# Kernel optimization log

Measured on AMD Instinct MI355X. Metric: run time of the kernel, lower is better.

The kernel has to match this reference:

```python
import jax, jax.numpy as jnp
import numpy as np
import math

B, N, C = 1, 2048, 256
H, CH = 8, 32
PQ, PV = 8, 12
CZ = 32
BQ, BK = 32, 128
NB = N // BQ
PAD = (BK - BQ) // 2
INF = 1e8
EPS = 1e-8

_KIDX = np.arange(NB)[:, None] * BQ + np.arange(BK)[None, :] - PAD
_KVALID = (_KIDX >= 0) & (_KIDX < N)
_KIDX_C = np.clip(_KIDX, 0, N - 1)


def _quat_to_rot(q):
    q = q / jnp.linalg.norm(q, axis=-1, keepdims=True)
    w, x, y, z = q[..., 0], q[..., 1], q[..., 2], q[..., 3]
    return jnp.stack([
        jnp.stack([1 - 2 * (y * y + z * z), 2 * (x * y - w * z), 2 * (x * z + w * y)], -1),
        jnp.stack([2 * (x * y + w * z), 1 - 2 * (x * x + z * z), 2 * (y * z - w * x)], -1),
        jnp.stack([2 * (x * z - w * y), 2 * (y * z + w * x), 1 - 2 * (x * x + y * y)], -1)], -2)


def _to_queries(x):
    # [B, N, ...] -> [B, NB, BQ, ...]
    return x.reshape((B, NB, BQ) + x.shape[2:])


def _to_keys(x):
    # [B, N, ...] -> [B, NB, BK, ...] zero-padded sliding key windows
    g = x[:, _KIDX_C]
    v = jnp.asarray(_KVALID, x.dtype).reshape((1, NB, BK) + (1,) * (x.ndim - 2))
    return g * v


def _ln(x):
    m = x.mean(-1, keepdims=True)
    var = x.var(-1, keepdims=True)
    return (x - m) / jnp.sqrt(var + 1e-5)


def setup_inputs():
    key = jax.random.key(0)
    ks = jax.random.split(key, 16)
    p = 0.02
    return {
        's': jax.random.normal(ks[0], (B, N, C), jnp.float32),
        'cond': jax.random.normal(ks[1], (B, N, C), jnp.float32),
        'z': jax.random.normal(ks[2], (B, NB, BQ, BK, CZ), jnp.float32),
        'trans': jax.random.normal(ks[3], (B, N, 3), jnp.float32),
        'rots': _quat_to_rot(jax.random.normal(ks[4], (B, N, 4), jnp.float32)),
        's_mask': jnp.ones((B, N), jnp.float32),
        'Wq': jax.random.normal(ks[5], (C, H * CH)) * p,
        'Wk': jax.random.normal(ks[6], (C, H * CH)) * p,
        'Wv': jax.random.normal(ks[7], (C, H * CH)) * p,
        'Wqp': jax.random.normal(ks[8], (C, H * PQ * 3)) * p,
        'Wkvp': jax.random.normal(ks[9], (C, H * (PQ + PV) * 3)) * p,
        'Wb': jax.random.normal(ks[10], (CZ, H)) * p,
        'Wdz': jax.random.normal(ks[11], (CZ, CZ // 4)) * p,
        'head_weights': jnp.full((H,), 0.5413),
        'Wout': jax.random.normal(ks[12], (H * (CZ // 4 + CH + PV * 4), C)) * p,
        'Wg': jax.random.normal(ks[13], (C, C)) * p,
        'bg': jnp.zeros((C,)),
        'Wbeta': jax.random.normal(ks[14], (C, C)) * p,
        'bbeta': jnp.zeros((C,)),
        'g_z': jnp.ones((CZ,)),
        'b_z': jnp.zeros((CZ,)),
    }


def reference(s, cond, z, trans, rots, s_mask, Wq, Wk, Wv, Wqp, Wkvp, Wb, Wdz,
              head_weights, Wout, Wg, bg, Wbeta, bbeta, g_z, b_z):
    # AdaLN on s conditioned on cond; LayerNorm on z
    s = _ln(s) * (cond @ Wg + bg) + (cond @ Wbeta + bbeta)
    z = _ln(z) * g_z + b_z

    q_in = _to_queries(s)            # [B,NB,BQ,C]
    k_in = _to_keys(s)               # [B,NB,BK,C]
    q_t = _to_queries(trans)         # [B,NB,BQ,3]
    q_R = _to_queries(rots)          # [B,NB,BQ,3,3]
    k_t = _to_keys(trans)
    k_R = _to_keys(rots)
    # zero-padded key rotations -> identity
    zero = jnp.all(k_R == 0, axis=(-2, -1))[..., None, None]
    k_R = jnp.where(zero, jnp.eye(3, dtype=k_R.dtype), k_R)

    q = (q_in @ Wq).reshape(B, NB, BQ, H, CH)
    k = (k_in @ Wk).reshape(B, NB, BK, H, CH)
    v = (k_in @ Wv).reshape(B, NB, BK, H, CH)

    q_pts = (q_in @ Wqp).reshape(B, NB, BQ, H * PQ, 3)
    q_pts = jnp.einsum('bnqij,bnqpj->bnqpi', q_R, q_pts) + q_t[..., None, :]
    q_pts = q_pts.reshape(B, NB, BQ, H, PQ, 3)

    kv_pts = (k_in @ Wkvp).reshape(B, NB, BK, H * (PQ + PV), 3)
    kv_pts = jnp.einsum('bnkij,bnkpj->bnkpi', k_R, kv_pts) + k_t[..., None, :]
    kv_pts = kv_pts.reshape(B, NB, BK, H, PQ + PV, 3)
    k_pts, v_pts = kv_pts[..., :PQ, :], kv_pts[..., PQ:, :]

    b = z @ Wb                                    # [B,NB,BQ,BK,H]
    a = jnp.einsum('bnqhc,bnkhc->bnqkh', q, k) * math.sqrt(1.0 / (3 * CH))
    a = a + math.sqrt(1.0 / 3.0) * b

    disp = q_pts[:, :, :, None] - k_pts[:, :, None]   # [B,NB,BQ,BK,H,PQ,3]
    d2 = jnp.sum(disp * disp, axis=-1)                # [B,NB,BQ,BK,H,PQ]
    hw = jax.nn.softplus(head_weights) * math.sqrt(1.0 / (3 * (PQ * 9.0 / 2)))
    pt_att = -0.5 * jnp.sum(d2 * hw[:, None], axis=-1)   # [B,NB,BQ,BK,H]

    m_q = _to_queries(s_mask[..., None])              # [B,NB,BQ,1]
    m_k = _to_keys(s_mask[..., None])                 # [B,NB,BK,1]
    attn_mask = m_q * jnp.swapaxes(m_k, -1, -2)       # [B,NB,BQ,BK]
    attn_mask = INF * (attn_mask - 1.0)

    a = a + pt_att + attn_mask[..., None]
    a = jnp.swapaxes(a, -1, -2)                       # [B,NB,BQ,H,BK]
    a = jax.nn.softmax(a, axis=-1)

    o = jnp.einsum('bnqhk,bnkhc->bnqhc', a, v).reshape(B, NB, BQ, H * CH)
    o_pt = jnp.einsum('bnqhk,bnkhvc->bnqhvc', a, v_pts)      # [B,NB,BQ,H,PV,3]
    o_pt = jnp.einsum('bnqji,bnqhvj->bnqhvi', q_R,
                      o_pt - q_t[:, :, :, None, None, :])     # invert apply
    o_pt_norm = jnp.sqrt(jnp.sum(o_pt ** 2, -1) + EPS).reshape(B, NB, BQ, H * PV)
    o_pt = o_pt.reshape(B, NB, BQ, H * PV * 3)
    pair_z = z @ Wdz                                          # [B,NB,BQ,BK,CZ//4]
    o_pair = jnp.einsum('bnqhk,bnqkc->bnqhc', a, pair_z).reshape(B, NB, BQ, H * (CZ // 4))

    out = jnp.concatenate([o, o_pt, o_pt_norm, o_pair], -1) @ Wout
    return out.reshape(B, N, C)
```

## Files before the change

kernel.cpp:

```cpp
#include <hip/hip_runtime.h>
#include <hip/hip_bf16.h>
#include <math.h>

typedef __hip_bfloat16 bf16;
typedef __attribute__((ext_vector_type(8))) short short8;
typedef __attribute__((ext_vector_type(4))) short short4v;
typedef __attribute__((ext_vector_type(4))) float f32x4;

#define NRES 2048
#define CDIM 256
#define PADK 48
#define POS 1440

static __device__ __forceinline__ float b2f(bf16 x) { return __bfloat162float(x); }
static __device__ __forceinline__ float us2f(short u) {
    return __uint_as_float(((unsigned)(unsigned short)u) << 16);
}
static __device__ __forceinline__ short f2s(float f) {
    bf16 h = __float2bfloat16(f);
    return *reinterpret_cast<short*>(&h);
}
static __device__ __forceinline__ bool flag_f32(const void* smask) {
    return *(const unsigned int*)smask == 0x3F800000u;
}
static __device__ __forceinline__ float dual_load(const void* p, size_t i, bool f32) {
    float vf = ((const float*)p)[f32 ? i : 0];
    float vb = b2f(((const bf16*)p)[f32 ? (size_t)0 : i]);
    return f32 ? vf : vb;
}

struct PrepTable {
    const void* src[8];
    bf16* dst[8];
    int srcN[8];
    int nOff[8];
    int dstStride[8];
    float scl[8];
    int tileOff[9];
    const void* s;
    const void* cond;
    bf16* condb;
    bf16* xnb;
    const void* rots;
    const void* trans;
    float* RT;
    const void* z;
    const void* Wb;
    const void* Wdz;
    const void* g_z;
    const void* b_z;
    bf16* Bzb;
    bf16* PZb;
};
__global__ __launch_bounds__(256) void k_prep(PrepTable tb, const void* __restrict__ smask) {
    __shared__ float tile[32][33];
    __shared__ float ls[8][CDIM];
    __shared__ float mrs[8][2];
    __shared__ float wb[32][8], wdz[32][8], gz[32], bz[32];
    bool f32 = flag_f32(smask);
    int b = blockIdx.x;
    int t = threadIdx.x;
    if (b < 1024) {
        {
            int j = t >> 3, c = t & 7;
            wb[j][c] = 0.5773502691896258f * dual_load(tb.Wb, t, f32);
            wdz[j][c] = dual_load(tb.Wdz, t, f32);
        }
        if (t < 32) { gz[t] = dual_load(tb.g_z, t, f32); bz[t] = dual_load(tb.b_z, t, f32); }
        __syncthreads();
        size_t r = (size_t)b * 256 + t;
        float zv[32];
        float sum = 0.f, sq = 0.f;
        if (f32) {
            const float4* zp = (const float4*)((const float*)tb.z + r * 32);
#pragma unroll
            for (int j4 = 0; j4 < 8; ++j4) {
                float4 v4 = zp[j4];
                zv[j4 * 4 + 0] = v4.x; zv[j4 * 4 + 1] = v4.y; zv[j4 * 4 + 2] = v4.z; zv[j4 * 4 + 3] = v4.w;
            }
        } else {
            const bf16* zp = (const bf16*)tb.z + r * 32;
#pragma unroll
            for (int j = 0; j < 32; ++j) zv[j] = b2f(zp[j]);
        }
#pragma unroll
        for (int j = 0; j < 32; ++j) { float v = zv[j]; sum += v; sq += v * v; }
        float m = sum / 32.f;
        float var = fmaxf(sq / 32.f - m * m, 0.f);
        float rstd = rsqrtf(var + 1e-5f);
#pragma unroll
        for (int j = 0; j < 32; ++j) zv[j] = (zv[j] - m) * rstd * gz[j] + bz[j];
        float bacc[8], pacc[8];
#pragma unroll
        for (int c = 0; c < 8; ++c) { bacc[c] = 0.f; pacc[c] = 0.f; }
        for (int j = 0; j < 32; ++j) {
            float v = zv[j];
#pragma unroll
            for (int c = 0; c < 8; ++c) { bacc[c] += v * wb[j][c]; pacc[c] += v * wdz[j][c]; }
        }
        int n = (int)(r >> 12);
        int q = (int)(r >> 7) & 31;
        int k = (int)r & 127;
#pragma unroll
        for (int h = 0; h < 8; ++h)
            tb.Bzb[(size_t)n * 32768 + (size_t)h * 4096 + q * 128 + k] = __float2bfloat16(bacc[h]);
#pragma unroll
        for (int c = 0; c < 8; ++c)
            tb.PZb[(((size_t)(n * 32 + q)) * 8 + c) * 128 + k] = __float2bfloat16(pacc[c]);
        return;
    }
    b -= 1024;
    if (b < tb.tileOff[8]) {
        int s = 0;
        while (b >= tb.tileOff[s + 1]) ++s;
        int rel = b - tb.tileOff[s];
        int ntTiles = tb.srcN[s] >> 5;
        int kt = rel / ntTiles, nt = rel % ntTiles;
        const void* src = tb.src[s];
        int srcN = tb.srcN[s];
        float scl = tb.scl[s];
        int tx = t & 31, ty = t >> 5;
#pragma unroll
        for (int r = 0; r < 4; ++r) {
            int srow = kt * 32 + ty + r * 8;
            int scol = nt * 32 + tx;
            tile[ty + r * 8][tx] = dual_load(src, (size_t)srow * srcN + scol, f32);
        }
        __syncthreads();
        bf16* dst = tb.dst[s];
#pragma unroll
        for (int r = 0; r < 4; ++r) {
            int n = nt * 32 + ty + r * 8 + tb.nOff[s];
            int k = kt * 32 + tx;
            dst[(size_t)n * tb.dstStride[s] + k] = __float2bfloat16(tile[tx][ty + r * 8] * scl);
        }
        return;
    }
    b -= tb.tileOff[8];
    if (b < 256) {
        int i0 = b * 2048;
        for (int i = t; i < 2048; i += 256)
            tb.condb[i0 + i] = __float2bfloat16(dual_load(tb.cond, (size_t)(i0 + i), f32));
        return;
    }
    b -= 256;
    if (b < 256) {
        int r0 = b * 8;
        for (int i = t; i < 8 * CDIM; i += 256) {
            int r = i >> 8, c = i & 255;
            ls[r][c] = dual_load(tb.s, (size_t)(r0 + r) * CDIM + c, f32);
        }
        __syncthreads();
        int wave = t >> 6, lane = t & 63;
        for (int rr = 0; rr < 2; ++rr) {
            int r = wave * 2 + rr;
            float sum = 0.f, sq = 0.f;
            for (int j = lane; j < CDIM; j += 64) { float v = ls[r][j]; sum += v; sq += v * v; }
            for (int off = 32; off; off >>= 1) { sum += __shfl_xor(sum, off); sq += __shfl_xor(sq, off); }
            if (lane == 0) {
                float m = sum / CDIM;
                float var = fmaxf(sq / CDIM - m * m, 0.f);
                mrs[r][0] = m; mrs[r][1] = rsqrtf(var + 1e-5f);
            }
        }
        __syncthreads();
        int c = t;
#pragma unroll
        for (int r = 0; r < 8; ++r)
            tb.xnb[(size_t)(r0 + r) * CDIM + c] = __float2bfloat16((ls[r][c] - mrs[r][0]) * mrs[r][1]);
        return;
    }
    b -= 256;
    int i = b * 256 + t;
    int row = i / 12, c = i % 12;
    float v = (c < 9) ? dual_load(tb.rots, (size_t)row * 9 + c, f32)
                      : dual_load(tb.trans, (size_t)row * 3 + (c - 9), f32);
    tb.RT[i] = v;
}

__global__ __launch_bounds__(256) void k_gb(
    const bf16* __restrict__ condb, const bf16* __restrict__ GWt, const bf16* __restrict__ xnb,
    const void* __restrict__ bg, const void* __restrict__ bbeta,
    const void* __restrict__ smask, bf16* __restrict__ SQb)
{
    bool f32 = flag_f32(smask);
    int wid = threadIdx.x >> 6, lane = threadIdx.x & 63;
    int tid = blockIdx.x * 4 + wid;
    int mt = tid >> 4, nt = tid & 15;
    int idx = lane & 15, quad = lane >> 4;
    const bf16* Ap = condb + (size_t)(mt * 16 + idx) * 256 + quad * 8;
    const bf16* B0 = GWt + (size_t)(nt * 16 + idx) * 256 + quad * 8;
    const bf16* B1 = GWt + (size_t)(256 + nt * 16 + idx) * 256 + quad * 8;
    f32x4 a0 = {0,0,0,0}, a1 = {0,0,0,0};
    for (int k = 0; k < 256; k += 32) {
        short8 af = *(const short8*)(Ap + k);
        a0 = __builtin_amdgcn_mfma_f32_16x16x32_bf16(af, *(const short8*)(B0 + k), a0, 0, 0, 0);
        a1 = __builtin_amdgcn_mfma_f32_16x16x32_bf16(af, *(const short8*)(B1 + k), a1, 0, 0, 0);
    }
    int ocol = nt * 16 + idx;
    float bgc = dual_load(bg, ocol, f32), bbc = dual_load(bbeta, ocol, f32);
    int orow = mt * 16 + quad * 4;
#pragma unroll
    for (int r = 0; r < 4; ++r) {
        int row = orow + r;
        float xn = b2f(xnb[(size_t)row * 256 + ocol]);
        SQb[(size_t)row * 256 + ocol] = __float2bfloat16(xn * (a0[r] + bgc) + (a1[r] + bbc));
    }
}

__global__ __launch_bounds__(256) void k_gemm22b(
    const bf16* __restrict__ A, const bf16* __restrict__ Bt, bf16* __restrict__ C,
    int N, int K, int totalWaves)
{
    int wid = threadIdx.x >> 6, lane = threadIdx.x & 63;
    int tid = blockIdx.x * 4 + wid;
    if (tid >= totalWaves) return;
    int tiles_n = N >> 5;
    int mt = tid / tiles_n, nt = tid % tiles_n;
    int idx = lane & 15, quad = lane >> 4;
    const bf16* Ap0 = A + (size_t)(mt * 32 + idx) * K + quad * 8;
    const bf16* Ap1 = Ap0 + (size_t)16 * K;
    const bf16* Bp0 = Bt + (size_t)(nt * 32 + idx) * K + quad * 8;
    const bf16* Bp1 = Bp0 + (size_t)16 * K;
    f32x4 a00 = {0,0,0,0}, a01 = {0,0,0,0}, a10 = {0,0,0,0}, a11 = {0,0,0,0};
    for (int k = 0; k < K; k += 32) {
        short8 af0 = *(const short8*)(Ap0 + k);
        short8 af1 = *(const short8*)(Ap1 + k);
        short8 bf0 = *(const short8*)(Bp0 + k);
        short8 bf1 = *(const short8*)(Bp1 + k);
        a00 = __builtin_amdgcn_mfma_f32_16x16x32_bf16(af0, bf0, a00, 0, 0, 0);
        a01 = __builtin_amdgcn_mfma_f32_16x16x32_bf16(af0, bf1, a01, 0, 0, 0);
        a10 = __builtin_amdgcn_mfma_f32_16x16x32_bf16(af1, bf0, a10, 0, 0, 0);
        a11 = __builtin_amdgcn_mfma_f32_16x16x32_bf16(af1, bf1, a11, 0, 0, 0);
    }
    int orow = mt * 32 + quad * 4;
    int ocol = nt * 32 + idx;
#pragma unroll
    for (int r = 0; r < 4; ++r) {
        C[(size_t)(orow + r) * N + ocol] = __float2bfloat16(a00[r]);
        C[(size_t)(orow + r) * N + ocol + 16] = __float2bfloat16(a01[r]);
        C[(size_t)(orow + r + 16) * N + ocol] = __float2bfloat16(a10[r]);
        C[(size_t)(orow + r + 16) * N + ocol + 16] = __float2bfloat16(a11[r]);
    }
}

__global__ __launch_bounds__(256) void k_attn_out(
    const bf16* __restrict__ POb,
    const bf16* __restrict__ Bzb, const bf16* __restrict__ PZb,
    const float* __restrict__ RT,
    const void* __restrict__ smask, const void* __restrict__ head_weights,
    bf16* __restrict__ CATb)
{
    __shared__ char buf[78720];
    __shared__ float rowq[32], rowk[128], mk[128], mqv[32];
    short* QfS = (short*)buf;
    short* KfS = (short*)(buf + 4608);
    short* VtS = (short*)(buf + 23040);
    short* AsS = (short*)(buf + 44800);
    float* S   = (float*)(buf + 53504);
    float* OPT = (float*)(buf + 53504);
    short* BzS = (short*)(buf + 70016);
    short* PtsS = (short*)(buf + 44800);
    short* QpS  = (short*)(buf + 62208);

    const int n = blockIdx.x >> 3, h = blockIdx.x & 7;
    const int t = threadIdx.x;
    const bool f32 = flag_f32(smask);
    const int n32 = n * 32;

    float hwv = dual_load(head_weights, h, f32);
    float ptc = -0.5f * log1pf(expf(hwv)) * 0.09622504486493764f;
    float m2ptc = -2.f * ptc;
    const short8 zero8 = {0,0,0,0,0,0,0,0};
    const short4v zero4 = {0,0,0,0};

    const int kR = t >> 1, halfR = t & 1;
    const int kgR = n32 + kR - PADK;
    const bool validR = (kgR >= 0 && kgR < NRES);
    float4 kr0, kr1, kr2;
    float kmv = 0.f;
    if (validR) {
        const float4* rt = (const float4*)(RT + (size_t)kgR * 12);
        kr0 = rt[0]; kr1 = rt[1]; kr2 = rt[2];
        if (halfR == 0) kmv = dual_load(smask, kgR, f32);
    }
    float4 qr0, qr1, qr2;
    float qmv = 0.f;
    if (t < 32) {
        const float4* rt = (const float4*)(RT + (size_t)(n32 + t) * 12);
        qr0 = rt[0]; qr1 = rt[1]; qr2 = rt[2];
        qmv = dual_load(smask, n32 + t, f32);
    }

    if (t < 128) {
        int q = t >> 2, g = t & 3;
        *(short8*)(QfS + q * 72 + g * 8) =
            *(const short8*)(POb + (size_t)(n32 + q) * POS + h * 32 + g * 8);
    }
    for (int i = t; i < 512; i += 256) {
        int k = i >> 2, g = i & 3;
        int kg = n32 + k - PADK;
        short8 v = zero8;
        if (kg >= 0 && kg < NRES)
            v = *(const short8*)(POb + (size_t)kg * POS + 256 + h * 32 + g * 8);
        *(short8*)(KfS + k * 72 + g * 8) = v;
    }
    for (int i = t; i < 512; i += 256) {
        int k = i >> 2, g = i & 3;
        int kg = n32 + k - PADK;
        short8 v = zero8;
        if (kg >= 0 && kg < NRES)
            v = *(const short8*)(POb + (size_t)kg * POS + 512 + h * 32 + g * 8);
#pragma unroll
        for (int j = 0; j < 8; ++j) VtS[(g * 8 + j) * 136 + k] = v[j];
    }
    {
        const short8* bsrc = (const short8*)(Bzb + (size_t)n * 32768 + (size_t)h * 4096);
        for (int i = t; i < 512; i += 256) {
            int row = i >> 4, g = i & 15;
            *(short8*)(BzS + row * 136 + g * 8) = bsrc[i];
        }
    }
    for (int i = t; i < 1920; i += 256) {
        int k = i / 15, g = i % 15;
        int kg = n32 + k - PADK;
        short4v v = zero4;
        if (kg >= 0 && kg < NRES)
            v = *(const short4v*)(POb + (size_t)kg * POS + 960 + h * 60 + g * 4);
        *(short4v*)(PtsS + k * 68 + g * 4) = v;
    }
    if (t < 192) {
        int q = t / 6, g = t % 6;
        *(short4v*)(QpS + q * 28 + g * 4) =
            *(const short4v*)(POb + (size_t)(n32 + q) * POS + 768 + h * 24 + g * 4);
    }
    for (int i = t; i < 320; i += 256) {
        if (i < 64) { int q = i >> 1, g = i & 1; *(short8*)(QfS + q * 72 + 56 + g * 8) = zero8; }
        else { int j = i - 64; int k = j >> 1, g = j & 1; *(short8*)(KfS + k * 72 + 56 + g * 8) = zero8; }
    }
    for (int i = t; i < 204; i += 256) {
        int r = 68 + i / 17, sg = i % 17;
        *(short8*)(VtS + r * 136 + sg * 8) = zero8;
    }
    __syncthreads();

    {
        if (validR) {
            float s2 = 0.f;
            int j0 = halfR * 10;
#pragma unroll
            for (int jj = 0; jj < 10; ++jj) {
                int j = j0 + jj;
                float x = us2f(PtsS[kR * 68 + j * 3 + 0]);
                float y = us2f(PtsS[kR * 68 + j * 3 + 1]);
                float z = us2f(PtsS[kR * 68 + j * 3 + 2]);
                float p0 = kr0.x * x + kr0.y * y + kr0.z * z + kr2.y;
                float p1 = kr0.w * x + kr1.x * y + kr1.y * z + kr2.z;
                float p2 = kr1.z * x + kr1.w * y + kr2.x * z + kr2.w;
                if (j < 8) {
                    KfS[kR * 72 + 32 + j * 3 + 0] = f2s(p0);
                    KfS[kR * 72 + 32 + j * 3 + 1] = f2s(p1);
                    KfS[kR * 72 + 32 + j * 3 + 2] = f2s(p2);
                    s2 += p0 * p0 + p1 * p1 + p2 * p2;
                } else {
                    int v = j - 8;
                    VtS[(32 + v * 3 + 0) * 136 + kR] = f2s(p0);
                    VtS[(32 + v * 3 + 1) * 136 + kR] = f2s(p1);
                    VtS[(32 + v * 3 + 2) * 136 + kR] = f2s(p2);
                }
            }
            if (halfR == 0) {
                rowk[kR] = ptc * s2;
                mk[kR] = kmv;
            }
        } else {
            if (halfR == 0) {
                for (int c = 32; c < 56; ++c) KfS[kR * 72 + c] = 0;
                for (int x = 32; x < 50; ++x) VtS[x * 136 + kR] = 0;
                rowk[kR] = 0.f; mk[kR] = 0.f;
            } else {
                for (int x = 50; x < 68; ++x) VtS[x * 136 + kR] = 0;
            }
        }
    }
    if (t < 32) {
        int q = t;
        mqv[q] = qmv;
        float s2 = 0.f;
#pragma unroll
        for (int p = 0; p < 8; ++p) {
            float x = us2f(QpS[q * 28 + p * 3 + 0]);
            float y = us2f(QpS[q * 28 + p * 3 + 1]);
            float z = us2f(QpS[q * 28 + p * 3 + 2]);
            float p0 = qr0.x * x + qr0.y * y + qr0.z * z + qr2.y;
            float p1 = qr0.w * x + qr1.x * y + qr1.y * z + qr2.z;
            float p2 = qr1.z * x + qr1.w * y + qr2.x * z + qr2.w;
            QfS[q * 72 + 32 + p * 3 + 0] = f2s(m2ptc * p0);
            QfS[q * 72 + 32 + p * 3 + 1] = f2s(m2ptc * p1);
            QfS[q * 72 + 32 + p * 3 + 2] = f2s(m2ptc * p2);
            s2 += p0 * p0 + p1 * p1 + p2 * p2;
        }
        rowq[q] = ptc * s2;
    }
    __syncthreads();

    const int wid = t >> 6, lane = t & 63, idx = lane & 15, quad = lane >> 4;
#pragma unroll
    for (int i = 0; i < 4; ++i) {
        int tt = wid * 4 + i;
        int mt = tt >> 3, nt = tt & 7;
        f32x4 acc = {0.f, 0.f, 0.f, 0.f};
#pragma unroll
        for (int kk = 0; kk < 2; ++kk) {
            short8 af  = *(const short8*)(QfS + (mt * 16 + idx) * 72 + kk * 32 + quad * 8);
            short8 bfv = *(const short8*)(KfS + (nt * 16 + idx) * 72 + kk * 32 + quad * 8);
            acc = __builtin_amdgcn_mfma_f32_16x16x32_bf16(af, bfv, acc, 0, 0, 0);
        }
#pragma unroll
        for (int r = 0; r < 4; ++r) {
            int q = mt * 16 + quad * 4 + r;
            int k = nt * 16 + idx;
            float bz = us2f(BzS[q * 136 + k]);
            float msk = 1e8f * (mqv[q] * mk[k] - 1.f);
            S[q * 129 + k] = acc[r] + bz + rowq[q] + rowk[k] + msk;
        }
    }
    __syncthreads();

    for (int rr = 0; rr < 8; ++rr) {
        int q = wid * 8 + rr;
        float v0 = S[q * 129 + lane], v1 = S[q * 129 + lane + 64];
        float mx = fmaxf(v0, v1);
        for (int off = 32; off; off >>= 1) mx = fmaxf(mx, __shfl_xor(mx, off));
        float e0 = expf(v0 - mx), e1 = expf(v1 - mx);
        float sm = e0 + e1;
        for (int off = 32; off; off >>= 1) sm += __shfl_xor(sm, off);
        float inv = 1.f / sm;
        AsS[q * 136 + lane] = f2s(e0 * inv);
        AsS[q * 136 + lane + 64] = f2s(e1 * inv);
    }
    __syncthreads();

    short8 pzr[16];
    {
        int q = t >> 3, c = t & 7;
        const short8* pzp = (const short8*)(PZb + ((size_t)(n32 + q) * 8 + c) * 128);
#pragma unroll
        for (int k8 = 0; k8 < 16; ++k8) pzr[k8] = pzp[k8];
    }
#pragma unroll
    for (int i = 0; i < 3; ++i) {
        int tt = wid + i * 4;
        if (tt >= 10) break;
        int mt = tt / 5, nt = tt % 5;
        f32x4 acc = {0.f, 0.f, 0.f, 0.f};
#pragma unroll
        for (int kk = 0; kk < 4; ++kk) {
            short8 af  = *(const short8*)(AsS + (mt * 16 + idx) * 136 + kk * 32 + quad * 8);
            short8 bfv = *(const short8*)(VtS + (nt * 16 + idx) * 136 + kk * 32 + quad * 8);
            acc = __builtin_amdgcn_mfma_f32_16x16x32_bf16(af, bfv, acc, 0, 0, 0);
        }
        int x = nt * 16 + idx;
#pragma unroll
        for (int r = 0; r < 4; ++r) {
            int q = mt * 16 + quad * 4 + r;
            if (x < 32)
                CATb[(size_t)(n32 + q) * 704 + h * 32 + x] = __float2bfloat16(acc[r]);
            else if (x < 68)
                OPT[q * 37 + (x - 32)] = acc[r];
        }
    }
    {
        int q = t >> 3, c = t & 7;
        const short8* asp = (const short8*)(AsS + q * 136);
        float acc = 0.f;
        for (int k8 = 0; k8 < 16; ++k8) {
            short8 pv = pzr[k8];
            short8 av = asp[k8];
#pragma unroll
            for (int j = 0; j < 8; ++j) acc += us2f(av[j]) * us2f(pv[j]);
        }
        CATb[(size_t)(n32 + q) * 704 + 640 + h * 8 + c] = __float2bfloat16(acc);
    }
    __syncthreads();

    for (int i = t; i < 384; i += 256) {
        int q = i / 12, v = i % 12;
        int g = n32 + q;
        const float4* rt = (const float4*)(RT + (size_t)g * 12);
        float4 r0 = rt[0], r1 = rt[1], r2 = rt[2];
        float x = OPT[q * 37 + v * 3 + 0] - r2.y;
        float y = OPT[q * 37 + v * 3 + 1] - r2.z;
        float z = OPT[q * 37 + v * 3 + 2] - r2.w;
        float o0 = r0.x * x + r0.w * y + r1.z * z;
        float o1 = r0.y * x + r1.x * y + r1.w * z;
        float o2 = r0.z * x + r1.y * y + r2.x * z;
        size_t cb = (size_t)g * 704;
        CATb[cb + 256 + (h * 12 + v) * 3 + 0] = __float2bfloat16(o0);
        CATb[cb + 256 + (h * 12 + v) * 3 + 1] = __float2bfloat16(o1);
        CATb[cb + 256 + (h * 12 + v) * 3 + 2] = __float2bfloat16(o2);
        CATb[cb + 544 + h * 12 + v] = __float2bfloat16(sqrtf(o0 * o0 + o1 * o1 + o2 * o2 + 1e-8f));
    }
}

__global__ __launch_bounds__(256) void k_gemm(
    const bf16* __restrict__ A, const bf16* __restrict__ Bt, void* __restrict__ Cv,
    int N, int K, int totalTiles, const void* __restrict__ smask)
{
    int wid = threadIdx.x >> 6, lane = threadIdx.x & 63;
    int tid = blockIdx.x * 4 + wid;
    if (tid >= totalTiles) return;
    int tiles_n = N >> 4;
    int mt = tid / tiles_n, nt = tid % tiles_n;
    int idx = lane & 15, quad = lane >> 4;
    const bf16* Ap = A + (size_t)(mt * 16 + idx) * K + quad * 8;
    const bf16* Bp = Bt + (size_t)(nt * 16 + idx) * K + quad * 8;
    f32x4 acc = {0.f, 0.f, 0.f, 0.f};
    for (int k = 0; k < K; k += 32) {
        short8 af = *(const short8*)(Ap + k);
        short8 bfv = *(const short8*)(Bp + k);
        acc = __builtin_amdgcn_mfma_f32_16x16x32_bf16(af, bfv, acc, 0, 0, 0);
    }
    int orow = mt * 16 + quad * 4;
    int ocol = nt * 16 + idx;
    if (flag_f32(smask)) {
        float* C = (float*)Cv;
#pragma unroll
        for (int r = 0; r < 4; ++r) C[(size_t)(orow + r) * N + ocol] = acc[r];
    } else {
        bf16* C = (bf16*)Cv;
#pragma unroll
        for (int r = 0; r < 4; ++r) C[(size_t)(orow + r) * N + ocol] = __float2bfloat16(acc[r]);
    }
}

extern "C" void kernel_launch(void* const* d_in, const int* in_sizes, int n_in,
                              void* d_out, int out_size, void* d_ws, size_t ws_size,
                              hipStream_t stream) {
    const void* s       = d_in[0];
    const void* cond    = d_in[1];
    const void* z       = d_in[2];
    const void* trans   = d_in[3];
    const void* rots    = d_in[4];
    const void* s_mask  = d_in[5];
    const void* Wq      = d_in[6];
    const void* Wk      = d_in[7];
    const void* Wv      = d_in[8];
    const void* Wqp     = d_in[9];
    const void* Wkvp    = d_in[10];
    const void* Wb      = d_in[11];
    const void* Wdz     = d_in[12];
    const void* hweights= d_in[13];
    const void* Wout    = d_in[14];
    const void* Wg      = d_in[15];
    const void* bg      = d_in[16];
    const void* Wbeta   = d_in[17];
    const void* bbeta   = d_in[18];
    const void* g_z     = d_in[19];
    const void* b_z     = d_in[20];

    float* ws = (float*)d_ws;
    bf16* POb   = (bf16*)(ws);
    bf16* Bzb   = (bf16*)(ws + 1474560);
    bf16* PZb   = (bf16*)(ws + 2523136);
    bf16* SQb   = (bf16*)(ws + 3571712);
    bf16* condb = (bf16*)(ws + 3833856);
    bf16* xnb   = (bf16*)(ws + 4096000);
    bf16* CATb  = (bf16*)(ws + 4358144);
    bf16* PWt   = (bf16*)(ws + 5079040);
    bf16* GWt   = (bf16*)(ws + 5263360);
    bf16* FWt   = (bf16*)(ws + 5328896);
    float* RT   = (float*)(ws + 5419008);

    PrepTable tb;
    const float qkscale = 0.10206207261596575f;
    tb.src[0] = Wq;   tb.dst[0] = PWt; tb.srcN[0] = 256; tb.nOff[0] = 0;   tb.dstStride[0] = 256; tb.scl[0] = qkscale;
    tb.src[1] = Wk;   tb.dst[1] = PWt; tb.srcN[1] = 256; tb.nOff[1] = 256; tb.dstStride[1] = 256; tb.scl[1] = 1.f;
    tb.src[2] = Wv;   tb.dst[2] = PWt; tb.srcN[2] = 256; tb.nOff[2] = 512; tb.dstStride[2] = 256; tb.scl[2] = 1.f;
    tb.src[3] = Wqp;  tb.dst[3] = PWt; tb.srcN[3] = 192; tb.nOff[3] = 768; tb.dstStride[3] = 256; tb.scl[3] = 1.f;
    tb.src[4] = Wkvp; tb.dst[4] = PWt; tb.srcN[4] = 480; tb.nOff[4] = 960; tb.dstStride[4] = 256; tb.scl[4] = 1.f;
    tb.src[5] = Wg;   tb.dst[5] = GWt; tb.srcN[5] = 256; tb.nOff[5] = 0;   tb.dstStride[5] = 256; tb.scl[5] = 1.f;
    tb.src[6] = Wbeta;tb.dst[6] = GWt; tb.srcN[6] = 256; tb.nOff[6] = 256; tb.dstStride[6] = 256; tb.scl[6] = 1.f;
    tb.src[7] = Wout; tb.dst[7] = FWt; tb.srcN[7] = 256; tb.nOff[7] = 0;   tb.dstStride[7] = 704; tb.scl[7] = 1.f;
    int tc[8] = {64, 64, 64, 48, 120, 64, 64, 176};
    tb.tileOff[0] = 0;
    for (int i = 0; i < 8; ++i) tb.tileOff[i + 1] = tb.tileOff[i] + tc[i];
    tb.s = s; tb.cond = cond; tb.condb = condb; tb.xnb = xnb;
    tb.rots = rots; tb.trans = trans; tb.RT = RT;
    tb.z = z; tb.Wb = Wb; tb.Wdz = Wdz; tb.g_z = g_z; tb.b_z = b_z;
    tb.Bzb = Bzb; tb.PZb = PZb;

    dim3 blk(256);
    k_prep<<<dim3(2296), blk, 0, stream>>>(tb, s_mask);
    k_gb<<<dim3(512), blk, 0, stream>>>(condb, GWt, xnb, bg, bbeta, s_mask, SQb);
    k_gemm22b<<<dim3(720), blk, 0, stream>>>(SQb, PWt, POb, 1440, 256, 2880);
    k_attn_out<<<dim3(512), blk, 0, stream>>>(POb, Bzb, PZb, RT, s_mask, hweights, CATb);
    k_gemm<<<dim3(512), blk, 0, stream>>>(CATb, FWt, d_out, 256, 704, 2048, s_mask);
}
```

Measured before the change: 175.4 us.

## Split attention blocks into half-query tiles with register-resident operands and smaller LDS

The attention kernel now launches one block per (window, head, half of the queries), doubling the grid to 1024 blocks and cutting shared memory from about 79KB to 39KB. Q/K feature fragments, pair-bias values and point coordinates are loaded straight into registers instead of being staged through LDS, and each key thread handles all 20 points. The aim is higher occupancy and fewer LDS round trips. The cost is that the V and key-point transforms are recomputed by both half-blocks, and an extra barrier is added so softmax results can be held in registers before the S buffer is reused.

```diff
diff --git a/kernel.cpp b/kernel.cpp
--- a/kernel.cpp
+++ b/kernel.cpp
@@ -251,60 +251,76 @@
     const void* __restrict__ smask, const void* __restrict__ head_weights,
     bf16* __restrict__ CATb)
 {
-    __shared__ char buf[78720];
-    __shared__ float rowq[32], rowk[128], mk[128], mqv[32];
-    short* QfS = (short*)buf;
-    short* KfS = (short*)(buf + 4608);
-    short* VtS = (short*)(buf + 23040);
-    short* AsS = (short*)(buf + 44800);
-    float* S   = (float*)(buf + 53504);
-    float* OPT = (float*)(buf + 53504);
-    short* BzS = (short*)(buf + 70016);
-    short* PtsS = (short*)(buf + 44800);
-    short* QpS  = (short*)(buf + 62208);
-
-    const int n = blockIdx.x >> 3, h = blockIdx.x & 7;
+    __shared__ char buf[39232];
+    __shared__ float rowq[16], rowk[128], mk[128], mqv[16];
+    short* VtS = (short*)buf;
+    short* KpS = (short*)(buf + 21760);
+    short* QpS = (short*)(buf + 29952);
+    float* S   = (float*)(buf + 30976);
+    short* AsS = (short*)(buf + 30976);
+    float* OPT = (float*)(buf + 35328);
+
+    const int bx = blockIdx.x;
+    const int n = bx >> 4, h = (bx >> 1) & 7, qh = bx & 1;
     const int t = threadIdx.x;
     const bool f32 = flag_f32(smask);
     const int n32 = n * 32;
+    const int q0 = qh * 16;
+    const int rowg = n32 + q0;
+
+    const int wid = t >> 6, lane = t & 63, idx = lane & 15, quad = lane >> 4;
 
     float hwv = dual_load(head_weights, h, f32);
     float ptc = -0.5f * log1pf(expf(hwv)) * 0.09622504486493764f;
     float m2ptc = -2.f * ptc;
     const short8 zero8 = {0,0,0,0,0,0,0,0};
-    const short4v zero4 = {0,0,0,0};
-
-    const int kR = t >> 1, halfR = t & 1;
-    const int kgR = n32 + kR - PADK;
-    const bool validR = (kgR >= 0 && kgR < NRES);
+
+    short8 afeat = *(const short8*)(POb + (size_t)(rowg + idx) * POS + h * 32 + quad * 8);
+    short8 bfeat[2];
+#pragma unroll
+    for (int i = 0; i < 2; ++i) {
+        int nt = wid * 2 + i;
+        int kg = n32 + nt * 16 + idx - PADK;
+        bfeat[i] = (kg >= 0 && kg < NRES)
+            ? *(const short8*)(POb + (size_t)kg * POS + 256 + h * 32 + quad * 8) : zero8;
+    }
+    short bzr[8];
+#pragma unroll
+    for (int i = 0; i < 2; ++i) {
+        int nt = wid * 2 + i;
+        int k = nt * 16 + idx;
+#pragma unroll
+        for (int r = 0; r < 4; ++r) {
+            int q = quad * 4 + r;
+            bzr[i * 4 + r] = *(const short*)(Bzb + (size_t)n * 32768 + (size_t)h * 4096 + (q0 + q) * 128 + k);
+        }
+    }
     float4 kr0, kr1, kr2;
     float kmv = 0.f;
+    short4v kpts[15];
+    const int kgR = n32 + t - PADK;
+    const bool validR = (t < 128) && (kgR >= 0 && kgR < NRES);
     if (validR) {
         const float4* rt = (const float4*)(RT + (size_t)kgR * 12);
         kr0 = rt[0]; kr1 = rt[1]; kr2 = rt[2];
-        if (halfR == 0) kmv = dual_load(smask, kgR, f32);
+        kmv = dual_load(smask, kgR, f32);
+        const short4v* pp = (const short4v*)(POb + (size_t)kgR * POS + 960 + h * 60);
+#pragma unroll
+        for (int g = 0; g < 15; ++g) kpts[g] = pp[g];
     }
     float4 qr0, qr1, qr2;
     float qmv = 0.f;
-    if (t < 32) {
-        const float4* rt = (const float4*)(RT + (size_t)(n32 + t) * 12);
+    short8 qpts[3];
+    if (t >= 240) {
+        int q = t - 240;
+        const float4* rt = (const float4*)(RT + (size_t)(rowg + q) * 12);
         qr0 = rt[0]; qr1 = rt[1]; qr2 = rt[2];
-        qmv = dual_load(smask, n32 + t, f32);
-    }
-
-    if (t < 128) {
-        int q = t >> 2, g = t & 3;
-        *(short8*)(QfS + q * 72 + g * 8) =
-            *(const short8*)(POb + (size_t)(n32 + q) * POS + h * 32 + g * 8);
-    }
-    for (int i = t; i < 512; i += 256) {
-        int k = i >> 2, g = i & 3;
-        int kg = n32 + k - PADK;
-        short8 v = zero8;
-        if (kg >= 0 && kg < NRES)
-            v = *(const short8*)(POb + (size_t)kg * POS + 256 + h * 32 + g * 8);
-        *(short8*)(KfS + k * 72 + g * 8) = v;
-    }
+        qmv = dual_load(smask, rowg + q, f32);
+        const short8* pp = (const short8*)(POb + (size_t)(rowg + q) * POS + 768 + h * 24);
+#pragma unroll
+        for (int g = 0; g < 3; ++g) qpts[g] = pp[g];
+    }
+
     for (int i = t; i < 512; i += 256) {
         int k = i >> 2, g = i & 3;
         int kg = n32 + k - PADK;
@@ -314,121 +330,85 @@
 #pragma unroll
         for (int j = 0; j < 8; ++j) VtS[(g * 8 + j) * 136 + k] = v[j];
     }
-    {
-        const short8* bsrc = (const short8*)(Bzb + (size_t)n * 32768 + (size_t)h * 4096);
-        for (int i = t; i < 512; i += 256) {
-            int row = i >> 4, g = i & 15;
-            *(short8*)(BzS + row * 136 + g * 8) = bsrc[i];
-        }
-    }
-    for (int i = t; i < 1920; i += 256) {
-        int k = i / 15, g = i % 15;
-        int kg = n32 + k - PADK;
-        short4v v = zero4;
-        if (kg >= 0 && kg < NRES)
-            v = *(const short4v*)(POb + (size_t)kg * POS + 960 + h * 60 + g * 4);
-        *(short4v*)(PtsS + k * 68 + g * 4) = v;
-    }
-    if (t < 192) {
-        int q = t / 6, g = t % 6;
-        *(short4v*)(QpS + q * 28 + g * 4) =
-            *(const short4v*)(POb + (size_t)(n32 + q) * POS + 768 + h * 24 + g * 4);
-    }
-    for (int i = t; i < 320; i += 256) {
-        if (i < 64) { int q = i >> 1, g = i & 1; *(short8*)(QfS + q * 72 + 56 + g * 8) = zero8; }
-        else { int j = i - 64; int k = j >> 1, g = j & 1; *(short8*)(KfS + k * 72 + 56 + g * 8) = zero8; }
-    }
-    for (int i = t; i < 204; i += 256) {
-        int r = 68 + i / 17, sg = i % 17;
-        *(short8*)(VtS + r * 136 + sg * 8) = zero8;
-    }
-    __syncthreads();
-
-    {
+    if (t < 128) {
+        int k = t;
         if (validR) {
+            const short* kp = (const short*)kpts;
             float s2 = 0.f;
-            int j0 = halfR * 10;
-#pragma unroll
-            for (int jj = 0; jj < 10; ++jj) {
-                int j = j0 + jj;
-                float x = us2f(PtsS[kR * 68 + j * 3 + 0]);
-                float y = us2f(PtsS[kR * 68 + j * 3 + 1]);
-                float z = us2f(PtsS[kR * 68 + j * 3 + 2]);
+#pragma unroll
+            for (int j = 0; j < 20; ++j) {
+                float x = us2f(kp[j * 3 + 0]);
+                float y = us2f(kp[j * 3 + 1]);
+                float z = us2f(kp[j * 3 + 2]);
                 float p0 = kr0.x * x + kr0.y * y + kr0.z * z + kr2.y;
                 float p1 = kr0.w * x + kr1.x * y + kr1.y * z + kr2.z;
                 float p2 = kr1.z * x + kr1.w * y + kr2.x * z + kr2.w;
                 if (j < 8) {
-                    KfS[kR * 72 + 32 + j * 3 + 0] = f2s(p0);
-                    KfS[kR * 72 + 32 + j * 3 + 1] = f2s(p1);
-                    KfS[kR * 72 + 32 + j * 3 + 2] = f2s(p2);
+                    KpS[k * 32 + j * 3 + 0] = f2s(p0);
+                    KpS[k * 32 + j * 3 + 1] = f2s(p1);
+                    KpS[k * 32 + j * 3 + 2] = f2s(p2);
                     s2 += p0 * p0 + p1 * p1 + p2 * p2;
                 } else {
                     int v = j - 8;
-                    VtS[(32 + v * 3 + 0) * 136 + kR] = f2s(p0);
-                    VtS[(32 + v * 3 + 1) * 136 + kR] = f2s(p1);
-                    VtS[(32 + v * 3 + 2) * 136 + kR] = f2s(p2);
+                    VtS[(32 + v * 3 + 0) * 136 + k] = f2s(p0);
+                    VtS[(32 + v * 3 + 1) * 136 + k] = f2s(p1);
+                    VtS[(32 + v * 3 + 2) * 136 + k] = f2s(p2);
                 }
             }
-            if (halfR == 0) {
-                rowk[kR] = ptc * s2;
-                mk[kR] = kmv;
-            }
+            *(short8*)(KpS + k * 32 + 24) = zero8;
+            rowk[k] = ptc * s2;
+            mk[k] = kmv;
         } else {
-            if (halfR == 0) {
-                for (int c = 32; c < 56; ++c) KfS[kR * 72 + c] = 0;
-                for (int x = 32; x < 50; ++x) VtS[x * 136 + kR] = 0;
-                rowk[kR] = 0.f; mk[kR] = 0.f;
-            } else {
-                for (int x = 50; x < 68; ++x) VtS[x * 136 + kR] = 0;
-            }
-        }
-    }
-    if (t < 32) {
-        int q = t;
-        mqv[q] = qmv;
+#pragma unroll
+            for (int g = 0; g < 4; ++g) *(short8*)(KpS + k * 32 + g * 8) = zero8;
+            for (int x = 32; x < 68; ++x) VtS[x * 136 + k] = 0;
+            rowk[k] = 0.f; mk[k] = 0.f;
+        }
+    } else if (t >= 240) {
+        int q = t - 240;
+        const short* qp = (const short*)qpts;
         float s2 = 0.f;
 #pragma unroll
         for (int p = 0; p < 8; ++p) {
-            float x = us2f(QpS[q * 28 + p * 3 + 0]);
-            float y = us2f(QpS[q * 28 + p * 3 + 1]);
-            float z = us2f(QpS[q * 28 + p * 3 + 2]);
+            float x = us2f(qp[p * 3 + 0]);
+            float y = us2f(qp[p * 3 + 1]);
+            float z = us2f(qp[p * 3 + 2]);
             float p0 = qr0.x * x + qr0.y * y + qr0.z * z + qr2.y;
             float p1 = qr0.w * x + qr1.x * y + qr1.y * z + qr2.z;
             float p2 = qr1.z * x + qr1.w * y + qr2.x * z + qr2.w;
-            QfS[q * 72 + 32 + p * 3 + 0] = f2s(m2ptc * p0);
-            QfS[q * 72 + 32 + p * 3 + 1] = f2s(m2ptc * p1);
-            QfS[q * 72 + 32 + p * 3 + 2] = f2s(m2ptc * p2);
+            QpS[q * 32 + p * 3 + 0] = f2s(m2ptc * p0);
+            QpS[q * 32 + p * 3 + 1] = f2s(m2ptc * p1);
+            QpS[q * 32 + p * 3 + 2] = f2s(m2ptc * p2);
             s2 += p0 * p0 + p1 * p1 + p2 * p2;
         }
+        *(short8*)(QpS + q * 32 + 24) = zero8;
         rowq[q] = ptc * s2;
+        mqv[q] = qmv;
     }
     __syncthreads();
 
-    const int wid = t >> 6, lane = t & 63, idx = lane & 15, quad = lane >> 4;
-#pragma unroll
-    for (int i = 0; i < 4; ++i) {
-        int tt = wid * 4 + i;
-        int mt = tt >> 3, nt = tt & 7;
+    short8 a2 = *(const short8*)(QpS + idx * 32 + quad * 8);
+#pragma unroll
+    for (int i = 0; i < 2; ++i) {
+        int nt = wid * 2 + i;
         f32x4 acc = {0.f, 0.f, 0.f, 0.f};
-#pragma unroll
-        for (int kk = 0; kk < 2; ++kk) {
-            short8 af  = *(const short8*)(QfS + (mt * 16 + idx) * 72 + kk * 32 + quad * 8);
-            short8 bfv = *(const short8*)(KfS + (nt * 16 + idx) * 72 + kk * 32 + quad * 8);
-            acc = __builtin_amdgcn_mfma_f32_16x16x32_bf16(af, bfv, acc, 0, 0, 0);
-        }
+        acc = __builtin_amdgcn_mfma_f32_16x16x32_bf16(afeat, bfeat[i], acc, 0, 0, 0);
+        short8 b2 = *(const short8*)(KpS + (nt * 16 + idx) * 32 + quad * 8);
+        acc = __builtin_amdgcn_mfma_f32_16x16x32_bf16(a2, b2, acc, 0, 0, 0);
+        int k = nt * 16 + idx;
 #pragma unroll
         for (int r = 0; r < 4; ++r) {
-            int q = mt * 16 + quad * 4 + r;
-            int k = nt * 16 + idx;
-            float bz = us2f(BzS[q * 136 + k]);
+            int q = quad * 4 + r;
             float msk = 1e8f * (mqv[q] * mk[k] - 1.f);
-            S[q * 129 + k] = acc[r] + bz + rowq[q] + rowk[k] + msk;
+            S[q * 129 + k] = acc[r] + us2f(bzr[i * 4 + r]) + rowq[q] + rowk[k] + msk;
         }
     }
     __syncthreads();
 
-    for (int rr = 0; rr < 8; ++rr) {
-        int q = wid * 8 + rr;
+    float sa0[4], sa1[4];
+#pragma unroll
+    for (int rr = 0; rr < 4; ++rr) {
+        int q = wid * 4 + rr;
         float v0 = S[q * 129 + lane], v1 = S[q * 129 + lane + 64];
         float mx = fmaxf(v0, v1);
         for (int off = 32; off; off >>= 1) mx = fmaxf(mx, __shfl_xor(mx, off));
@@ -436,41 +416,47 @@
         float sm = e0 + e1;
         for (int off = 32; off; off >>= 1) sm += __shfl_xor(sm, off);
         float inv = 1.f / sm;
-        AsS[q * 136 + lane] = f2s(e0 * inv);
-        AsS[q * 136 + lane + 64] = f2s(e1 * inv);
+        sa0[rr] = e0 * inv; sa1[rr] = e1 * inv;
     }
     __syncthreads();
+#pragma unroll
+    for (int rr = 0; rr < 4; ++rr) {
+        int q = wid * 4 + rr;
+        AsS[q * 136 + lane] = f2s(sa0[rr]);
+        AsS[q * 136 + lane + 64] = f2s(sa1[rr]);
+    }
+    __syncthreads();
 
     short8 pzr[16];
-    {
+    if (t < 128) {
         int q = t >> 3, c = t & 7;
-        const short8* pzp = (const short8*)(PZb + ((size_t)(n32 + q) * 8 + c) * 128);
+        const short8* pzp = (const short8*)(PZb + ((size_t)(rowg + q) * 8 + c) * 128);
 #pragma unroll
         for (int k8 = 0; k8 < 16; ++k8) pzr[k8] = pzp[k8];
     }
 #pragma unroll
-    for (int i = 0; i < 3; ++i) {
+    for (int i = 0; i < 2; ++i) {
         int tt = wid + i * 4;
-        if (tt >= 10) break;
-        int mt = tt / 5, nt = tt % 5;
+        if (tt >= 5) break;
+        int nt = tt;
         f32x4 acc = {0.f, 0.f, 0.f, 0.f};
 #pragma unroll
         for (int kk = 0; kk < 4; ++kk) {
-            short8 af  = *(const short8*)(AsS + (mt * 16 + idx) * 136 + kk * 32 + quad * 8);
+            short8 af  = *(const short8*)(AsS + idx * 136 + kk * 32 + quad * 8);
             short8 bfv = *(const short8*)(VtS + (nt * 16 + idx) * 136 + kk * 32 + quad * 8);
             acc = __builtin_amdgcn_mfma_f32_16x16x32_bf16(af, bfv, acc, 0, 0, 0);
         }
         int x = nt * 16 + idx;
 #pragma unroll
         for (int r = 0; r < 4; ++r) {
-            int q = mt * 16 + quad * 4 + r;
+            int q = quad * 4 + r;
             if (x < 32)
-                CATb[(size_t)(n32 + q) * 704 + h * 32 + x] = __float2bfloat16(acc[r]);
+                CATb[(size_t)(rowg + q) * 704 + h * 32 + x] = __float2bfloat16(acc[r]);
             else if (x < 68)
                 OPT[q * 37 + (x - 32)] = acc[r];
         }
     }
-    {
+    if (t < 128) {
         int q = t >> 3, c = t & 7;
         const short8* asp = (const short8*)(AsS + q * 136);
         float acc = 0.f;
@@ -480,13 +466,13 @@
 #pragma unroll
             for (int j = 0; j < 8; ++j) acc += us2f(av[j]) * us2f(pv[j]);
         }
-        CATb[(size_t)(n32 + q) * 704 + 640 + h * 8 + c] = __float2bfloat16(acc);
+        CATb[(size_t)(rowg + q) * 704 + 640 + h * 8 + c] = __float2bfloat16(acc);
     }
     __syncthreads();
 
-    for (int i = t; i < 384; i += 256) {
-        int q = i / 12, v = i % 12;
-        int g = n32 + q;
+    if (t < 192) {
+        int q = t / 12, v = t % 12;
+        int g = rowg + q;
         const float4* rt = (const float4*)(RT + (size_t)g * 12);
         float4 r0 = rt[0], r1 = rt[1], r2 = rt[2];
         float x = OPT[q * 37 + v * 3 + 0] - r2.y;
@@ -594,6 +580,6 @@
     k_prep<<<dim3(2296), blk, 0, stream>>>(tb, s_mask);
     k_gb<<<dim3(512), blk, 0, stream>>>(condb, GWt, xnb, bg, bbeta, s_mask, SQb);
     k_gemm22b<<<dim3(720), blk, 0, stream>>>(SQb, PWt, POb, 1440, 256, 2880);
-    k_attn_out<<<dim3(512), blk, 0, stream>>>(POb, Bzb, PZb, RT, s_mask, hweights, CATb);
+    k_attn_out<<<dim3(1024), blk, 0, stream>>>(POb, Bzb, PZb, RT, s_mask, hweights, CATb);
     k_gemm<<<dim3(512), blk, 0, stream>>>(CATb, FWt, d_out, 256, 704, 2048, s_mask);
 }
```

After: 170.2 us. -3.0%, faster.
